# Kernel tuning notes

Measured on AMD Instinct MI355X. Metric: run time of the kernel, lower is better.

The kernel has to match this reference:

```python
import jax, jax.numpy as jnp
import numpy as np

LEAK = 0.95
EPS = 1e-4
THRESH = 1.0


def spike_fn(x):
    # forward of SurrogateBPFunction: heaviside(x > 0)
    return (x > 0).astype(x.dtype)


def setup_inputs() -> dict:
    key = jax.random.key(0)
    k1, k2, k3 = jax.random.split(key, 3)
    T, B, D_in, H, C = 20, 512, 4096, 1024, 100
    z = jax.random.normal(k1, (T, B, D_in), dtype=jnp.float32)
    # xavier_uniform with gain=2: bound = 2 * sqrt(6/(fan_in+fan_out))
    b1 = 2.0 * np.sqrt(6.0 / (D_in + H))
    W1 = jax.random.uniform(k2, (H, D_in), dtype=jnp.float32, minval=-b1, maxval=b1)
    b2 = 2.0 * np.sqrt(6.0 / (H + C))
    W2 = jax.random.uniform(k3, (C, H), dtype=jnp.float32, minval=-b2, maxval=b2)
    bn_gamma = jnp.ones((T, H), dtype=jnp.float32)
    return {"z": z, "W1": W1, "bn_gamma": bn_gamma, "W2": W2}


def reference(z, W1, bn_gamma, W2):
    T = z.shape[0]
    B = z.shape[1]
    H = W1.shape[0]
    C = W2.shape[0]

    def step(carry, xs):
        mem1, mem2 = carry
        inp_t, gamma = xs  # inp_t: [B, D_in], gamma: [H]
        h = jnp.einsum('bd,hd->bh', inp_t, W1)  # fc1, no bias
        # BatchNorm1d (training-mode batch stats, affine weight, no bias)
        mean = h.mean(axis=0)
        var = h.var(axis=0)  # biased variance, matches torch BN
        h = gamma * (h - mean) * jax.lax.rsqrt(var + EPS)
        mem1 = LEAK * mem1 + h
        mem_thr = mem1 / THRESH - 1.0
        out = spike_fn(mem_thr)
        rst = jnp.where(mem_thr > 0, THRESH, 0.0).astype(mem1.dtype)
        mem1 = mem1 - rst
        mem2 = mem2 + jnp.einsum('bh,ch->bc', out, W2)
        return (mem1, mem2), None

    mem1_0 = jnp.zeros((B, H), dtype=z.dtype)
    mem2_0 = jnp.zeros((B, C), dtype=z.dtype)
    (mem1, mem2), _ = jax.lax.scan(step, (mem1_0, mem2_0), (z, bn_gamma))
    return mem2 / T
```

## Files before the change

### kernel.cpp

```cpp
#include <hip/hip_runtime.h>
#include <hip/hip_bf16.h>
#include <stdint.h>

typedef _Float16 half8 __attribute__((ext_vector_type(8)));
typedef _Float16 half4v __attribute__((ext_vector_type(4)));
typedef float f32x4 __attribute__((ext_vector_type(4)));

#define T_STEPS 20
#define B_SZ 512
#define D_IN 4096
#define H_SZ 1024
#define C_SZ 100
#define M_TOT (T_STEPS * B_SZ)
#define BK 32

__device__ __forceinline__ void gload16(const _Float16* g, _Float16* l) {
  __builtin_amdgcn_global_load_lds(
      (const __attribute__((address_space(1))) void*)g,
      (__attribute__((address_space(3))) void*)l, 16, 0, 0);
}

struct HL {
  half8 h;
  half8 l;
};
__device__ __forceinline__ HL split8(float4 a, float4 b) {
  HL r;
  auto p0 = __builtin_amdgcn_cvt_pkrtz(a.x, a.y);
  auto p1 = __builtin_amdgcn_cvt_pkrtz(a.z, a.w);
  auto p2 = __builtin_amdgcn_cvt_pkrtz(b.x, b.y);
  auto p3 = __builtin_amdgcn_cvt_pkrtz(b.z, b.w);
  r.h[0] = p0.x; r.h[1] = p0.y; r.h[2] = p1.x; r.h[3] = p1.y;
  r.h[4] = p2.x; r.h[5] = p2.y; r.h[6] = p3.x; r.h[7] = p3.y;
  auto q0 = __builtin_amdgcn_cvt_pkrtz(a.x - (float)p0.x, a.y - (float)p0.y);
  auto q1 = __builtin_amdgcn_cvt_pkrtz(a.z - (float)p1.x, a.w - (float)p1.y);
  auto q2 = __builtin_amdgcn_cvt_pkrtz(b.x - (float)p2.x, b.y - (float)p2.y);
  auto q3 = __builtin_amdgcn_cvt_pkrtz(b.z - (float)p3.x, b.w - (float)p3.y);
  r.l[0] = q0.x; r.l[1] = q0.y; r.l[2] = q1.x; r.l[3] = q1.y;
  r.l[4] = q2.x; r.l[5] = q2.y; r.l[6] = q3.x; r.l[7] = q3.y;
  return r;
}

__global__ void k_split4(const float* __restrict__ x, _Float16* __restrict__ hi,
                         _Float16* __restrict__ lo) {
  int64_t i = (int64_t)blockIdx.x * blockDim.x + threadIdx.x;
  float4 v = ((const float4* __restrict__)x)[i];
  half4v h, l;
  h.x = (_Float16)v.x; l.x = (_Float16)(v.x - (float)h.x);
  h.y = (_Float16)v.y; l.y = (_Float16)(v.y - (float)h.y);
  h.z = (_Float16)v.z; l.z = (_Float16)(v.z - (float)h.z);
  h.w = (_Float16)v.w; l.w = (_Float16)(v.w - (float)h.w);
  ((half4v*)hi)[i] = h;
  ((half4v*)lo)[i] = l;
}

__global__ void k_prep_w2(const float* __restrict__ w2, _Float16* __restrict__ hi,
                          _Float16* __restrict__ lo) {
  int i = blockIdx.x * 256 + threadIdx.x;
  float v = (i < C_SZ * H_SZ) ? w2[i] : 0.0f;
  _Float16 h = (_Float16)v;
  hi[i] = h;
  lo[i] = (_Float16)(v - (float)h);
}

__global__ __launch_bounds__(256) void k_gemm1(
    const float* __restrict__ Z,
    const _Float16* __restrict__ Whi, const _Float16* __restrict__ Wlo,
    float* __restrict__ Hbuf) {
  __shared__ _Float16 sAh[4096];
  __shared__ _Float16 sAl[4096];
  __shared__ _Float16 sWh[4096];
  __shared__ _Float16 sWl[4096];

  const int tid = threadIdx.x;
  const int lane = tid & 63;
  const int w = tid >> 6;

  const int bid = blockIdx.x;
  const int xcd = bid & 7;
  const int q = bid >> 3;
  const int mt = xcd * 10 + (q >> 3);
  const int nt = q & 7;
  const int64_t m0 = (int64_t)mt * 128;
  const int64_t n0 = (int64_t)nt * 128;

  const int sfr = tid & 15;
  const int sq = (tid >> 4) & 3;
  const float* gz = Z + (m0 + (int64_t)(w * 16 + sfr)) * D_IN + sq * 8;
  const int aws = w * 512 + (sq * 16 + sfr) * 8;

  const _Float16* gW = Whi + (n0 + (int64_t)(w * 16 + (lane & 15))) * D_IN + (lane >> 4) * 8;
  const _Float16* gWl2 = Wlo + (n0 + (int64_t)(w * 16 + (lane & 15))) * D_IN + (lane >> 4) * 8;
  const int wws = w * 512 + lane * 8;
  const int64_t g2w = (int64_t)64 * D_IN;

  const int wm = (w >> 1) * 64;
  const int wn = (w & 1) * 64;
  const int ra = (wm >> 4) * 512 + lane * 8;
  const int rb = (wn >> 4) * 512 + lane * 8;
  const int fr = lane & 15;
  const int quad = lane >> 4;

  f32x4 acc[4][4] = {};

  float4 r00 = *(const float4*)(gz);
  float4 r01 = *(const float4*)(gz + 4);
  float4 r10 = *(const float4*)(gz + g2w);
  float4 r11 = *(const float4*)(gz + g2w + 4);

  for (int kt = 0; kt < D_IN; kt += BK) {
    __syncthreads();

    gload16(gW + kt, &sWh[wws]);
    gload16(gW + kt + g2w, &sWh[wws + 2048]);
    gload16(gWl2 + kt, &sWl[wws]);
    gload16(gWl2 + kt + g2w, &sWl[wws + 2048]);

    {
      HL p0 = split8(r00, r01);
      *(half8*)&sAh[aws] = p0.h;
      *(half8*)&sAl[aws] = p0.l;
      HL p1 = split8(r10, r11);
      *(half8*)&sAh[aws + 2048] = p1.h;
      *(half8*)&sAl[aws + 2048] = p1.l;
    }

    __syncthreads();

    if (kt + BK < D_IN) {
      r00 = *(const float4*)(gz + kt + BK);
      r01 = *(const float4*)(gz + kt + BK + 4);
      r10 = *(const float4*)(gz + kt + BK + g2w);
      r11 = *(const float4*)(gz + kt + BK + g2w + 4);
    }

    half8 ah[4], al[4], bh[4], bl[4];
#pragma unroll
    for (int i = 0; i < 4; ++i) {
      ah[i] = *(const half8*)&sAh[ra + i * 512];
      al[i] = *(const half8*)&sAl[ra + i * 512];
    }
#pragma unroll
    for (int j = 0; j < 4; ++j) {
      bh[j] = *(const half8*)&sWh[rb + j * 512];
      bl[j] = *(const half8*)&sWl[rb + j * 512];
    }
#pragma unroll
    for (int i = 0; i < 4; ++i) {
#pragma unroll
      for (int j = 0; j < 4; ++j) {
        acc[i][j] = __builtin_amdgcn_mfma_f32_16x16x32_f16(ah[i], bh[j], acc[i][j], 0, 0, 0);
        acc[i][j] = __builtin_amdgcn_mfma_f32_16x16x32_f16(ah[i], bl[j], acc[i][j], 0, 0, 0);
        acc[i][j] = __builtin_amdgcn_mfma_f32_16x16x32_f16(al[i], bh[j], acc[i][j], 0, 0, 0);
      }
    }
  }

#pragma unroll
  for (int i = 0; i < 4; ++i) {
#pragma unroll
    for (int r = 0; r < 4; ++r) {
      const int64_t row = m0 + wm + i * 16 + quad * 4 + r;
      float* dst = Hbuf + row * H_SZ + n0 + wn + fr;
#pragma unroll
      for (int j = 0; j < 4; ++j) dst[j * 16] = acc[i][j][r];
    }
  }
}

__global__ void k_stats(const float* __restrict__ Hbuf, const float* __restrict__ gamma,
                        float* __restrict__ scale, float* __restrict__ shift) {
  const int t = blockIdx.y;
  const int tx = threadIdx.x & 15;
  const int ty = threadIdx.x >> 4;
  const int h = blockIdx.x * 16 + tx;
  const float* p = Hbuf + ((int64_t)t * B_SZ + ty * 32) * H_SZ + h;
  float s = 0.f, s2 = 0.f;
#pragma unroll 8
  for (int i = 0; i < 32; ++i) {
    float v = p[(int64_t)i * H_SZ];
    s += v;
    s2 += v * v;
  }
  __shared__ float ss[16][16];
  __shared__ float sq[16][16];
  ss[ty][tx] = s;
  sq[ty][tx] = s2;
  __syncthreads();
  if (ty == 0) {
    float a = 0.f, b = 0.f;
#pragma unroll
    for (int k = 0; k < 16; ++k) {
      a += ss[k][tx];
      b += sq[k][tx];
    }
    const float mean = a * (1.0f / B_SZ);
    const float var = b * (1.0f / B_SZ) - mean * mean;
    const float rs = rsqrtf(var + 1e-4f);
    const float sc = gamma[t * H_SZ + h] * rs;
    scale[t * H_SZ + h] = sc;
    shift[t * H_SZ + h] = -mean * sc;
  }
}

__global__ void k_recur(const float* __restrict__ Hbuf, const float* __restrict__ scale,
                        const float* __restrict__ shift, _Float16* __restrict__ S) {
  const int idx = blockIdx.x * 256 + threadIdx.x;
  const int b = idx >> 10;
  const int h = idx & 1023;
  float mem = 0.f;
  int cnt = 0;
#pragma unroll
  for (int t = 0; t < T_STEPS; ++t) {
    float v = Hbuf[((int64_t)(t * B_SZ + b) << 10) + h];
    v = v * scale[(t << 10) + h] + shift[(t << 10) + h];
    mem = 0.95f * mem + v;
    if (mem - 1.0f > 0.0f) {
      ++cnt;
      mem -= 1.0f;
    }
  }
  S[idx] = (_Float16)cnt;
}

__global__ void k_gemm2(const _Float16* __restrict__ S, const _Float16* __restrict__ W2h,
                        const _Float16* __restrict__ W2l, float* __restrict__ out) {
  const int wid = threadIdx.x >> 6;
  const int lane = threadIdx.x & 63;
  const int m0 = blockIdx.y * 64 + wid * 16;
  const int n0 = blockIdx.x * 16;
  const int fr = lane & 15;
  const int quad = lane >> 4;

  const _Float16* sp = S + (int64_t)(m0 + fr) * H_SZ + quad * 8;
  const _Float16* wph = W2h + (int64_t)(n0 + fr) * H_SZ + quad * 8;
  const _Float16* wpl = W2l + (int64_t)(n0 + fr) * H_SZ + quad * 8;

  f32x4 acc = {0.f, 0.f, 0.f, 0.f};
#pragma unroll 4
  for (int k = 0; k < H_SZ; k += 32) {
    half8 a = *(const half8*)(sp + k);
    half8 bh = *(const half8*)(wph + k);
    half8 bl = *(const half8*)(wpl + k);
    acc = __builtin_amdgcn_mfma_f32_16x16x32_f16(a, bh, acc, 0, 0, 0);
    acc = __builtin_amdgcn_mfma_f32_16x16x32_f16(a, bl, acc, 0, 0, 0);
  }
  const int col = n0 + fr;
  if (col < C_SZ) {
#pragma unroll
    for (int r = 0; r < 4; ++r) {
      const int row = m0 + quad * 4 + r;
      out[row * C_SZ + col] = acc[r] * (1.0f / T_STEPS);
    }
  }
}

extern "C" void kernel_launch(void* const* d_in, const int* in_sizes, int n_in,
                              void* d_out, int out_size, void* d_ws, size_t ws_size,
                              hipStream_t stream) {
  const float* z = (const float*)d_in[0];
  const float* W1 = (const float*)d_in[1];
  const float* gamma = (const float*)d_in[2];
  const float* W2 = (const float*)d_in[3];
  float* out = (float*)d_out;

  char* ws = (char*)d_ws;
  size_t off = 0;
  auto alloc = [&](size_t bytes) -> void* {
    void* p = ws + off;
    off += (bytes + 255) & ~(size_t)255;
    return p;
  };
  _Float16* Whi = (_Float16*)alloc((size_t)H_SZ * D_IN * 2);
  _Float16* Wlo = (_Float16*)alloc((size_t)H_SZ * D_IN * 2);
  float* Hbuf = (float*)alloc((size_t)M_TOT * H_SZ * 4);
  float* scale = (float*)alloc((size_t)T_STEPS * H_SZ * 4);
  float* shift = (float*)alloc((size_t)T_STEPS * H_SZ * 4);
  _Float16* S = (_Float16*)alloc((size_t)B_SZ * H_SZ * 2);
  _Float16* W2h = (_Float16*)alloc((size_t)112 * H_SZ * 2);
  _Float16* W2l = (_Float16*)alloc((size_t)112 * H_SZ * 2);

  k_split4<<<(H_SZ * D_IN) / 1024, 256, 0, stream>>>(W1, Whi, Wlo);
  k_prep_w2<<<(112 * H_SZ) / 256, 256, 0, stream>>>(W2, W2h, W2l);

  k_gemm1<<<640, 256, 0, stream>>>(z, Whi, Wlo, Hbuf);

  dim3 gs(H_SZ / 16, T_STEPS);
  k_stats<<<gs, 256, 0, stream>>>(Hbuf, gamma, scale, shift);

  k_recur<<<(B_SZ * H_SZ) / 256, 256, 0, stream>>>(Hbuf, scale, shift, S);

  dim3 g2(7, 8);
  k_gemm2<<<g2, 256, 0, stream>>>(S, W2h, W2l, out);
}
```

Baseline: 591.3 us.

## Double-buffer W tiles in gemm1 and widen stats kernel row coverage

```diff
diff --git a/kernel.cpp b/kernel.cpp
--- a/kernel.cpp
+++ b/kernel.cpp
@@ -13,6 +13,7 @@
 #define C_SZ 100
 #define M_TOT (T_STEPS * B_SZ)
 #define BK 32
+#define KITERS (D_IN / BK)
 
 __device__ __forceinline__ void gload16(const _Float16* g, _Float16* l) {
   __builtin_amdgcn_global_load_lds(
@@ -69,8 +70,8 @@
     float* __restrict__ Hbuf) {
   __shared__ _Float16 sAh[4096];
   __shared__ _Float16 sAl[4096];
-  __shared__ _Float16 sWh[4096];
-  __shared__ _Float16 sWl[4096];
+  __shared__ _Float16 sWh[8192];
+  __shared__ _Float16 sWl[8192];
 
   const int tid = threadIdx.x;
   const int lane = tid & 63;
@@ -103,18 +104,17 @@
 
   f32x4 acc[4][4] = {};
 
+  gload16(gW, &sWh[wws]);
+  gload16(gW + g2w, &sWh[wws + 2048]);
+  gload16(gWl2, &sWl[wws]);
+  gload16(gWl2 + g2w, &sWl[wws + 2048]);
   float4 r00 = *(const float4*)(gz);
   float4 r01 = *(const float4*)(gz + 4);
   float4 r10 = *(const float4*)(gz + g2w);
   float4 r11 = *(const float4*)(gz + g2w + 4);
 
-  for (int kt = 0; kt < D_IN; kt += BK) {
+  for (int i = 0; i < KITERS; ++i) {
     __syncthreads();
-
-    gload16(gW + kt, &sWh[wws]);
-    gload16(gW + kt + g2w, &sWh[wws + 2048]);
-    gload16(gWl2 + kt, &sWl[wws]);
-    gload16(gWl2 + kt + g2w, &sWl[wws + 2048]);
 
     {
       HL p0 = split8(r00, r01);
@@ -127,43 +127,47 @@
 
     __syncthreads();
 
-    if (kt + BK < D_IN) {
-      r00 = *(const float4*)(gz + kt + BK);
-      r01 = *(const float4*)(gz + kt + BK + 4);
-      r10 = *(const float4*)(gz + kt + BK + g2w);
-      r11 = *(const float4*)(gz + kt + BK + g2w + 4);
-    }
-
+    const int woff = ((i + 1) & 1) * 4096;
+    if (i + 1 < KITERS) {
+      const int kt = (i + 1) * BK;
+      gload16(gW + kt, &sWh[woff + wws]);
+      gload16(gW + kt + g2w, &sWh[woff + wws + 2048]);
+      gload16(gWl2 + kt, &sWl[woff + wws]);
+      gload16(gWl2 + kt + g2w, &sWl[woff + wws + 2048]);
+      r00 = *(const float4*)(gz + kt);
+      r01 = *(const float4*)(gz + kt + 4);
+      r10 = *(const float4*)(gz + kt + g2w);
+      r11 = *(const float4*)(gz + kt + g2w + 4);
+    }
+
+    const int wcur = (i & 1) * 4096;
     half8 ah[4], al[4], bh[4], bl[4];
 #pragma unroll
-    for (int i = 0; i < 4; ++i) {
-      ah[i] = *(const half8*)&sAh[ra + i * 512];
-      al[i] = *(const half8*)&sAl[ra + i * 512];
-    }
-#pragma unroll
     for (int j = 0; j < 4; ++j) {
-      bh[j] = *(const half8*)&sWh[rb + j * 512];
-      bl[j] = *(const half8*)&sWl[rb + j * 512];
-    }
-#pragma unroll
-    for (int i = 0; i < 4; ++i) {
-#pragma unroll
-      for (int j = 0; j < 4; ++j) {
-        acc[i][j] = __builtin_amdgcn_mfma_f32_16x16x32_f16(ah[i], bh[j], acc[i][j], 0, 0, 0);
-        acc[i][j] = __builtin_amdgcn_mfma_f32_16x16x32_f16(ah[i], bl[j], acc[i][j], 0, 0, 0);
-        acc[i][j] = __builtin_amdgcn_mfma_f32_16x16x32_f16(al[i], bh[j], acc[i][j], 0, 0, 0);
+      ah[j] = *(const half8*)&sAh[ra + j * 512];
+      al[j] = *(const half8*)&sAl[ra + j * 512];
+      bh[j] = *(const half8*)&sWh[wcur + rb + j * 512];
+      bl[j] = *(const half8*)&sWl[wcur + rb + j * 512];
+    }
+#pragma unroll
+    for (int a = 0; a < 4; ++a) {
+#pragma unroll
+      for (int b = 0; b < 4; ++b) {
+        acc[a][b] = __builtin_amdgcn_mfma_f32_16x16x32_f16(ah[a], bh[b], acc[a][b], 0, 0, 0);
+        acc[a][b] = __builtin_amdgcn_mfma_f32_16x16x32_f16(ah[a], bl[b], acc[a][b], 0, 0, 0);
+        acc[a][b] = __builtin_amdgcn_mfma_f32_16x16x32_f16(al[a], bh[b], acc[a][b], 0, 0, 0);
       }
     }
   }
 
 #pragma unroll
-  for (int i = 0; i < 4; ++i) {
+  for (int a = 0; a < 4; ++a) {
 #pragma unroll
     for (int r = 0; r < 4; ++r) {
-      const int64_t row = m0 + wm + i * 16 + quad * 4 + r;
+      const int64_t row = m0 + wm + a * 16 + quad * 4 + r;
       float* dst = Hbuf + row * H_SZ + n0 + wn + fr;
 #pragma unroll
-      for (int j = 0; j < 4; ++j) dst[j * 16] = acc[i][j][r];
+      for (int b = 0; b < 4; ++b) dst[b * 16] = acc[a][b][r];
     }
   }
 }
@@ -171,29 +175,25 @@
 __global__ void k_stats(const float* __restrict__ Hbuf, const float* __restrict__ gamma,
                         float* __restrict__ scale, float* __restrict__ shift) {
   const int t = blockIdx.y;
-  const int tx = threadIdx.x & 15;
-  const int ty = threadIdx.x >> 4;
-  const int h = blockIdx.x * 16 + tx;
-  const float* p = Hbuf + ((int64_t)t * B_SZ + ty * 32) * H_SZ + h;
+  const int tx = threadIdx.x & 63;
+  const int ty = threadIdx.x >> 6;
+  const int h = blockIdx.x * 64 + tx;
+  const float* p = Hbuf + ((int64_t)t * B_SZ + ty * 128) * H_SZ + h;
   float s = 0.f, s2 = 0.f;
 #pragma unroll 8
-  for (int i = 0; i < 32; ++i) {
+  for (int i = 0; i < 128; ++i) {
     float v = p[(int64_t)i * H_SZ];
     s += v;
     s2 += v * v;
   }
-  __shared__ float ss[16][16];
-  __shared__ float sq[16][16];
+  __shared__ float ss[4][64];
+  __shared__ float sq[4][64];
   ss[ty][tx] = s;
   sq[ty][tx] = s2;
   __syncthreads();
   if (ty == 0) {
-    float a = 0.f, b = 0.f;
-#pragma unroll
-    for (int k = 0; k < 16; ++k) {
-      a += ss[k][tx];
-      b += sq[k][tx];
-    }
+    float a = ss[0][tx] + ss[1][tx] + ss[2][tx] + ss[3][tx];
+    float b = sq[0][tx] + sq[1][tx] + sq[2][tx] + sq[3][tx];
     const float mean = a * (1.0f / B_SZ);
     const float var = b * (1.0f / B_SZ) - mean * mean;
     const float rs = rsqrtf(var + 1e-4f);
@@ -285,7 +285,7 @@
 
   k_gemm1<<<640, 256, 0, stream>>>(z, Whi, Wlo, Hbuf);
 
-  dim3 gs(H_SZ / 16, T_STEPS);
+  dim3 gs(H_SZ / 64, T_STEPS);
   k_stats<<<gs, 256, 0, stream>>>(Hbuf, gamma, scale, shift);
 
   k_recur<<<(B_SZ * H_SZ) / 256, 256, 0, stream>>>(Hbuf, scale, shift, S);
```

After: 789.1 us. 1.33x slower.
